# Optimization experiments

Hardware: AMD Instinct MI355X
Metric: run time of the kernel (lower is better)

The kernel has to match this reference:

```python
import jax, jax.numpy as jnp
import numpy as np

NQ = 16
DIM = 1 << NQ
NUM_BLOCKS = 2
TOTAL_PARAMS = 78  # per weight_shapes; only first 48 consumed by the circuit


def _apply_1q(state, w, U):
    # state: (B, DIM); U: (2,2) shared or (B,2,2) per-sample
    B = state.shape[0]
    s = state.reshape(B, 1 << w, 2, 1 << (NQ - 1 - w))
    if U.ndim == 2:
        out = jnp.einsum('ij,bljr->blir', U, s)
    else:
        out = jnp.einsum('bij,bljr->blir', U, s)
    return out.reshape(B, DIM)


def _apply_2q(state, a, b, U):
    # a < b always in this circuit; U: (4,4)
    B = state.shape[0]
    Ut = U.reshape(2, 2, 2, 2)
    s = state.reshape(B, 1 << a, 2, 1 << (b - a - 1), 2, 1 << (NQ - 1 - b))
    out = jnp.einsum('ijkl,bxkylz->bxiyjz', Ut, s)
    return out.reshape(B, DIM)


def _rx(t):
    c = jnp.cos(t / 2).astype(jnp.complex64)
    s = (-1j * jnp.sin(t / 2)).astype(jnp.complex64)
    return jnp.stack([jnp.stack([c, s], -1), jnp.stack([s, c], -1)], -2)


def _ry(t):
    c = jnp.cos(t / 2).astype(jnp.complex64)
    s = jnp.sin(t / 2).astype(jnp.complex64)
    return jnp.stack([jnp.stack([c, -s], -1), jnp.stack([s, c], -1)], -2)


def _rz(t):
    em = jnp.exp(-1j * t.astype(jnp.complex64) / 2)
    ep = jnp.exp(1j * t.astype(jnp.complex64) / 2)
    z = jnp.zeros_like(em)
    return jnp.stack([jnp.stack([em, z], -1), jnp.stack([z, ep], -1)], -2)


def _ising_xx(t):
    c = jnp.cos(t / 2).astype(jnp.complex64)
    m = (-1j * jnp.sin(t / 2)).astype(jnp.complex64)
    z = jnp.zeros((), jnp.complex64)
    return jnp.array([[c, z, z, m], [z, c, m, z], [z, m, c, z], [m, z, z, c]])


def _ising_yy(t):
    c = jnp.cos(t / 2).astype(jnp.complex64)
    m = (-1j * jnp.sin(t / 2)).astype(jnp.complex64)
    p = (1j * jnp.sin(t / 2)).astype(jnp.complex64)
    z = jnp.zeros((), jnp.complex64)
    return jnp.array([[c, z, z, p], [z, c, m, z], [z, m, c, z], [p, z, z, c]])


def _ising_zz(t):
    em = jnp.exp(-1j * t.astype(jnp.complex64) / 2)
    ep = jnp.exp(1j * t.astype(jnp.complex64) / 2)
    z = jnp.zeros((), jnp.complex64)
    return jnp.array([[em, z, z, z], [z, ep, z, z], [z, z, ep, z], [z, z, z, em]])


_H = (jnp.array([[1, 1], [1, -1]], jnp.complex64) / np.sqrt(2).astype(np.float32))
_CZ = jnp.diag(jnp.array([1, 1, 1, -1], jnp.complex64))
_CNOT = jnp.array([[1, 0, 0, 0], [0, 1, 0, 0], [0, 0, 0, 1], [0, 0, 1, 0]], jnp.complex64)


def _circuit(x, weights):
    B = x.shape[0]
    state = jnp.zeros((B, DIM), jnp.complex64).at[:, 0].set(1.0)
    # state preparation
    for q in range(NQ):
        state = _apply_1q(state, q, _H)
    for q in range(NQ - 1):
        state = _apply_2q(state, q, q + 1, _CZ)
    # feature encoding (per-sample angles)
    for q in range(NQ):
        ang = x[:, q]
        state = _apply_1q(state, q, _rx(ang))
        state = _apply_1q(state, q, _ry(ang))
        state = _apply_1q(state, q, _rz(ang))
    # conv + pool blocks
    qubits = list(range(NQ))
    idx = 0
    for _ in range(NUM_BLOCKS):
        npairs = len(qubits) // 2
        cw = weights[idx:idx + npairs * 3].reshape(npairs, 3)
        idx += npairs * 3
        for w_idx, i in enumerate(range(0, len(qubits) - 1, 2)):
            a, b = qubits[i], qubits[i + 1]
            state = _apply_2q(state, a, b, _ising_xx(cw[w_idx, 0]))
            state = _apply_2q(state, a, b, _ising_yy(cw[w_idx, 1]))
            state = _apply_2q(state, a, b, _ising_zz(cw[w_idx, 2]))
        nkeep = len(qubits) // 2
        pw = weights[idx:idx + nkeep]
        idx += nkeep
        new_q = []
        for i in range(0, len(qubits), 2):
            ctrl, tgt = qubits[i], qubits[i + 1]
            state = _apply_2q(state, ctrl, tgt, _CNOT)
            state = _apply_1q(state, ctrl, _ry(pw[i // 2]))
            new_q.append(ctrl)
        qubits = new_q
    # <Z> on surviving qubits [0,4,8,12]
    probs = state.real ** 2 + state.imag ** 2
    outs = []
    for q in qubits:
        p = probs.reshape(B, 1 << q, 2, -1)
        outs.append(p[:, :, 0, :].sum((1, 2)) - p[:, :, 1, :].sum((1, 2)))
    return jnp.stack(outs, -1)  # (B, 4)


def setup_inputs() -> dict:
    key = jax.random.key(0)
    k1, k2, k3 = jax.random.split(key, 3)
    x = jax.random.normal(k1, (32, NQ), jnp.float32)
    weights = 0.1 * jax.random.normal(k2, (TOTAL_PARAMS,), jnp.float32)
    W = 0.1 * jax.random.normal(k3, (9, 4), jnp.float32)  # Linear(4, 9)
    b = jnp.zeros((9,), jnp.float32)
    return {"x": x, "weights": weights, "W": W, "b": b}


def reference(x, weights, W, b):
    q_out = _circuit(x, weights)  # (B, 4) real
    return q_out @ W.T + b  # (B, 9)
```

## Files before the change

### kernel.cpp

```cpp
#include <hip/hip_runtime.h>
#include <math.h>


struct C { float x, y; };
__device__ __forceinline__ C operator+(C a, C b){ return {a.x+b.x, a.y+b.y}; }
__device__ __forceinline__ C operator-(C a, C b){ return {a.x-b.x, a.y-b.y}; }
__device__ __forceinline__ C cmul(C a, C b){ return { a.x*b.x - a.y*b.y, a.x*b.y + a.y*b.x }; }
__device__ __forceinline__ C cfma(C a, C b, C acc){
  acc.x = fmaf(a.x, b.x, fmaf(-a.y, b.y, acc.x));
  acc.y = fmaf(a.x, b.y, fmaf( a.y, b.x, acc.y));
  return acc;
}
__device__ __forceinline__ C cfmac(C a, C b, C acc){
  acc.x = fmaf(a.x, b.x, fmaf( a.y, b.y, acc.x));
  acc.y = fmaf(a.y, b.x, fmaf(-a.x, b.y, acc.y));
  return acc;
}
__device__ __forceinline__ C cscale(C a, float s){ return {a.x*s, a.y*s}; }

__global__ __launch_bounds__(256) void qk_all(const float* __restrict__ x,
                                              const float* __restrict__ w,
                                              const float* __restrict__ Wm,
                                              const float* __restrict__ bias,
                                              float* __restrict__ outp)
{
  __shared__ C G[12][16];
  __shared__ C uL[64];
  __shared__ C sV[1024];
  __shared__ C sT[256];
  __shared__ C sM[256];
  __shared__ C sDp[64];
  __shared__ C sDz[64];
  __shared__ float qv[4];

  const int tid = threadIdx.x;
  const int b   = blockIdx.x;

  {
    int p = tid >> 4;
    if (p < 12) {
      int idx = tid & 15, r = idx >> 2, c = idx & 3;
      float a0, a1, a2, ry;
      if (p < 8) { a0 = w[3*p];   a1 = w[3*p+1];  a2 = w[3*p+2];  ry = w[24+p]; }
      else { int n = p-8; a0 = w[32+3*n]; a1 = w[33+3*n]; a2 = w[34+3*n]; ry = w[44+n]; }
      float s0,c0,s1,c1,s2,c2,sr,cr;
      sincosf(0.5f*a0, &s0, &c0);
      sincosf(0.5f*a1, &s1, &c1);
      sincosf(0.5f*a2, &s2, &c2);
      sincosf(0.5f*ry, &sr, &cr);
      int rlo = r & 1, rhi = r >> 1;
      float d   = rlo ? fmaf(-s0, s1, c0*c1) : fmaf(s0, s1, c0*c1);
      float eps = rlo ? fmaf( c0, s1, c1*s0) : fmaf(-c0, s1, c1*s0);
      bool valid = rlo ? (c == 1 || c == 2) : (c == 0 || c == 3);
      bool sel   = rlo ? (c == 2) : (c == 3);
      float re, im;
      if (!sel) { re = rhi ?  sr*d : cr*d;  im = rhi ? -cr*eps :  sr*eps; }
      else      { re = rhi ?  cr*d : -sr*d; im = rhi ? -sr*eps : -cr*eps; }
      float zi = rlo ? s2 : -s2;
      C val;
      if (valid) val = { fmaf(re, c2, -im*zi), fmaf(re, zi, im*c2) };
      else       val = {0.f, 0.f};
      G[p][idx] = val;
    } else if (tid >= 192 && tid < 208) {
      int q = tid - 192;
      float h = 0.5f * x[b*16 + q];
      float s, c;
      sincosf(h, &s, &c);
      C em = {c,-s}, ep = {c,s};
      C A00 = { c*c,  s*s}, A01 = {-c*s, -c*s};
      C A10 = { c*s, -c*s}, A11 = { c*c, -s*s};
      uL[q*4+0] = cmul(em, A00);
      uL[q*4+1] = cmul(em, A01);
      uL[q*4+2] = cmul(ep, A10);
      uL[q*4+3] = cmul(ep, A11);
    }
  }
  __syncthreads();

  {
    int lp = tid >> 4, lc = tid & 15;
    int p3=(lp>>3)&1, p2=(lp>>2)&1, p1=(lp>>1)&1, p0=lp&1;
    int l3=(lc>>3)&1, l2=(lc>>2)&1, l1=(lc>>1)&1, l0=lc&1;
    for (int n=0;n<4;n++){
      C acc{0,0};
      #pragma unroll
      for (int m3=0;m3<2;m3++)
      #pragma unroll
      for (int m1=0;m1<2;m1++){
        C g2 = G[8+n]  [(p3*2+p1)*4 + (m3*2+m1)];
        C ga = G[2*n]  [(m3*2+p2)*4 + (l3*2+l2)];
        C gb = G[2*n+1][(m1*2+p0)*4 + (l1*2+l0)];
        acc = cfma(g2, cmul(ga, gb), acc);
      }
      sV[n*256 + lp*16 + lc] = acc;
    }
  }
  if (tid < 64) {
    int n = tid >> 4, s = tid & 15;
    int t0 = (s>>3)&1;
    C u0 = uL[(4*n)*4 + t0*2 + 0], u1 = uL[(4*n)*4 + t0*2 + 1];
    C P00=u0, P01=u0, P10=u1, P11={-u1.x,-u1.y};
    #pragma unroll
    for (int i=1;i<4;i++){
      int t = (s >> (3-i)) & 1;
      int q = 4*n + i;
      C v0 = uL[q*4 + t*2 + 0], v1 = uL[q*4 + t*2 + 1];
      C b00, b01, b10, b11;
      if (n == 3 && i == 3) { b00=v0; b01={0,0}; b10=v1; b11={0,0}; }
      else { b00=v0; b01=v0; b10=v1; b11={-v1.x,-v1.y}; }
      C n00 = cfma(P01, b10, cmul(P00, b00));
      C n01 = cfma(P01, b11, cmul(P00, b01));
      C n10 = cfma(P11, b10, cmul(P10, b00));
      C n11 = cfma(P11, b11, cmul(P10, b01));
      P00=n00; P01=n01; P10=n10; P11=n11;
    }
    int base = tid << 2;
    sT[base+0]=P00; sT[base+1]=P01; sT[base+2]=P10; sT[base+3]=P11;
  }
  __syncthreads();

  {
    int n = tid >> 6, s = (tid >> 2) & 15, ab = tid & 3;
    const C* vr = &sV[n*256 + s*16];
    const C* tn = &sT[(n<<6) + ab];
    C acc{0,0};
    #pragma unroll
    for (int k=0;k<16;k++) acc = cfma(vr[k], tn[k<<2], acc);
    sM[tid] = acc;
  }
  __syncthreads();

  if (tid < 64) {
    int n = tid >> 4, p = tid & 15;
    int a=(p>>3)&1, a2=(p>>2)&1, bb=(p>>1)&1, b2=p&1;
    const C* mn = &sM[n<<6];
    C Slo{0,0}, Shi{0,0};
    #pragma unroll
    for (int s=0;s<8;s++)  Slo = cfmac(mn[(s<<2)+(a<<1)+bb], mn[(s<<2)+(a2<<1)+b2], Slo);
    #pragma unroll
    for (int s=8;s<16;s++) Shi = cfmac(mn[(s<<2)+(a<<1)+bb], mn[(s<<2)+(a2<<1)+b2], Shi);
    sDp[tid] = Slo + Shi;
    sDz[tid] = Slo - Shi;
  }
  __syncthreads();

  if (tid < 4) {
    int o = tid;
    C v0={1,0}, v1={1,0}, v2={1,0}, v3={1,0};
    #pragma unroll
    for (int n=0;n<3;n++){
      const C* D = (n==o) ? &sDz[n<<4] : &sDp[n<<4];
      C n0{0,0}, n1{0,0}, n2{0,0}, n3{0,0};
      n0 = cfma(v0, D[ 0], n0); n0 = cfma(v1, D[ 4], n0); n0 = cfma(v2, D[ 8], n0); n0 = cfma(v3, D[12], n0);
      n1 = cfma(v0, D[ 1], n1); n1 = cfma(v1, D[ 5], n1); n1 = cfma(v2, D[ 9], n1); n1 = cfma(v3, D[13], n1);
      n2 = cfma(v0, D[ 2], n2); n2 = cfma(v1, D[ 6], n2); n2 = cfma(v2, D[10], n2); n2 = cfma(v3, D[14], n2);
      n3 = cfma(v0, D[ 3], n3); n3 = cfma(v1, D[ 7], n3); n3 = cfma(v2, D[11], n3); n3 = cfma(v3, D[15], n3);
      v0=n0; v1=n1; v2=n2; v3=n3;
    }
    const C* D3 = (o==3) ? &sDz[3<<4] : &sDp[3<<4];
    C e{0,0};
    e = cfma(v0, D3[ 0], e); e = cfma(v1, D3[ 4], e);
    e = cfma(v2, D3[ 8], e); e = cfma(v3, D3[12], e);
    qv[o] = e.x * (1.0f/65536.0f);
  }
  __syncthreads();

  if (tid < 9) {
    float acc = bias[tid];
    #pragma unroll
    for (int k=0;k<4;k++) acc = fmaf(qv[k], Wm[tid*4+k], acc);
    outp[b*9 + tid] = acc;
  }
}

extern "C" void kernel_launch(void* const* d_in, const int* in_sizes, int n_in,
                              void* d_out, int out_size, void* d_ws, size_t ws_size,
                              hipStream_t stream)
{
  (void)in_sizes; (void)n_in; (void)out_size; (void)d_ws; (void)ws_size;
  const float* x    = (const float*)d_in[0];
  const float* w    = (const float*)d_in[1];
  const float* Wm   = (const float*)d_in[2];
  const float* bias = (const float*)d_in[3];
  float* outp = (float*)d_out;

  qk_all<<<32, 256, 0, stream>>>(x, w, Wm, bias, outp);
}
```

Measured before the change: 9.584 us.

## Factor per-block contraction into half-products and parallelize reduction stages

Replaces the 1024-entry sV tensor plus product-state sT contraction with a factored scheme. It builds 128 half-block partial products sH, then forms sM directly from the G[8+n] gate and pairs of half products, cutting arithmetic and shared memory. The density reduction is split across 128 threads by low/high half, and the final chain runs on 16 lanes with shuffles instead of 4 serial threads. It also switches to fast __sincosf intrinsics, which trades some accuracy for cheaper transcendentals.

```diff
diff --git a/kernel.cpp b/kernel.cpp
--- a/kernel.cpp
+++ b/kernel.cpp
@@ -16,7 +16,6 @@
   acc.y = fmaf(a.y, b.x, fmaf(-a.x, b.y, acc.y));
   return acc;
 }
-__device__ __forceinline__ C cscale(C a, float s){ return {a.x*s, a.y*s}; }
 
 __global__ __launch_bounds__(256) void qk_all(const float* __restrict__ x,
                                               const float* __restrict__ w,
@@ -26,11 +25,10 @@
 {
   __shared__ C G[12][16];
   __shared__ C uL[64];
-  __shared__ C sV[1024];
-  __shared__ C sT[256];
+  __shared__ C sH[128];
   __shared__ C sM[256];
-  __shared__ C sDp[64];
-  __shared__ C sDz[64];
+  __shared__ C sSlo[64];
+  __shared__ C sShi[64];
   __shared__ float qv[4];
 
   const int tid = threadIdx.x;
@@ -44,10 +42,10 @@
       if (p < 8) { a0 = w[3*p];   a1 = w[3*p+1];  a2 = w[3*p+2];  ry = w[24+p]; }
       else { int n = p-8; a0 = w[32+3*n]; a1 = w[33+3*n]; a2 = w[34+3*n]; ry = w[44+n]; }
       float s0,c0,s1,c1,s2,c2,sr,cr;
-      sincosf(0.5f*a0, &s0, &c0);
-      sincosf(0.5f*a1, &s1, &c1);
-      sincosf(0.5f*a2, &s2, &c2);
-      sincosf(0.5f*ry, &sr, &cr);
+      __sincosf(0.5f*a0, &s0, &c0);
+      __sincosf(0.5f*a1, &s1, &c1);
+      __sincosf(0.5f*a2, &s2, &c2);
+      __sincosf(0.5f*ry, &sr, &cr);
       int rlo = r & 1, rhi = r >> 1;
       float d   = rlo ? fmaf(-s0, s1, c0*c1) : fmaf(s0, s1, c0*c1);
       float eps = rlo ? fmaf( c0, s1, c1*s0) : fmaf(-c0, s1, c1*s0);
@@ -65,7 +63,7 @@
       int q = tid - 192;
       float h = 0.5f * x[b*16 + q];
       float s, c;
-      sincosf(h, &s, &c);
+      __sincosf(h, &s, &c);
       C em = {c,-s}, ep = {c,s};
       C A00 = { c*c,  s*s}, A01 = {-c*s, -c*s};
       C A10 = { c*s, -c*s}, A11 = { c*c, -s*s};
@@ -77,91 +75,94 @@
   }
   __syncthreads();
 
-  {
-    int lp = tid >> 4, lc = tid & 15;
-    int p3=(lp>>3)&1, p2=(lp>>2)&1, p1=(lp>>1)&1, p0=lp&1;
-    int l3=(lc>>3)&1, l2=(lc>>2)&1, l1=(lc>>1)&1, l0=lc&1;
-    for (int n=0;n<4;n++){
-      C acc{0,0};
-      #pragma unroll
-      for (int m3=0;m3<2;m3++)
-      #pragma unroll
-      for (int m1=0;m1<2;m1++){
-        C g2 = G[8+n]  [(p3*2+p1)*4 + (m3*2+m1)];
-        C ga = G[2*n]  [(m3*2+p2)*4 + (l3*2+l2)];
-        C gb = G[2*n+1][(m1*2+p0)*4 + (l1*2+l0)];
-        acc = cfma(g2, cmul(ga, gb), acc);
+  if (tid < 128) {
+    int n = tid >> 5, side = (tid >> 4) & 1, u = (tid >> 2) & 3;
+    int a = (tid >> 1) & 1, bb = tid & 1;
+    int q1 = 4*n + 2*side;
+    bool chat = (n == 3 && side == 1);
+    float t1 = a ? -1.f : 1.f;
+    float coef = (chat || !bb) ? t1 : -t1;
+    bool zero = chat && bb;
+    const C* g1 = &G[2*n + side][u*4];
+    C acc{0,0};
+    #pragma unroll
+    for (int v=0; v<4; v++){
+      C pv{0,0};
+      if (!zero) {
+        int thi = v >> 1, tlo = v & 1;
+        C u1a = uL[q1*4 + thi*2 + a];
+        C u20 = uL[q1*4 + 4 + tlo*2 + 0];
+        C u21 = uL[q1*4 + 4 + tlo*2 + 1];
+        C inner = { fmaf(coef, u21.x, u20.x), fmaf(coef, u21.y, u20.y) };
+        pv = cmul(u1a, inner);
       }
-      sV[n*256 + lp*16 + lc] = acc;
+      acc = cfma(g1[v], pv, acc);
     }
-  }
-  if (tid < 64) {
-    int n = tid >> 4, s = tid & 15;
-    int t0 = (s>>3)&1;
-    C u0 = uL[(4*n)*4 + t0*2 + 0], u1 = uL[(4*n)*4 + t0*2 + 1];
-    C P00=u0, P01=u0, P10=u1, P11={-u1.x,-u1.y};
-    #pragma unroll
-    for (int i=1;i<4;i++){
-      int t = (s >> (3-i)) & 1;
-      int q = 4*n + i;
-      C v0 = uL[q*4 + t*2 + 0], v1 = uL[q*4 + t*2 + 1];
-      C b00, b01, b10, b11;
-      if (n == 3 && i == 3) { b00=v0; b01={0,0}; b10=v1; b11={0,0}; }
-      else { b00=v0; b01=v0; b10=v1; b11={-v1.x,-v1.y}; }
-      C n00 = cfma(P01, b10, cmul(P00, b00));
-      C n01 = cfma(P01, b11, cmul(P00, b01));
-      C n10 = cfma(P11, b10, cmul(P10, b00));
-      C n11 = cfma(P11, b11, cmul(P10, b01));
-      P00=n00; P01=n01; P10=n10; P11=n11;
-    }
-    int base = tid << 2;
-    sT[base+0]=P00; sT[base+1]=P01; sT[base+2]=P10; sT[base+3]=P11;
+    sH[tid] = acc;
   }
   __syncthreads();
 
   {
-    int n = tid >> 6, s = (tid >> 2) & 15, ab = tid & 3;
-    const C* vr = &sV[n*256 + s*16];
-    const C* tn = &sT[(n<<6) + ab];
+    int n = tid >> 6, s = (tid >> 2) & 15;
+    int a = (tid >> 1) & 1, bb = tid & 1;
+    int s3=(s>>3)&1, s2b=(s>>2)&1, s1=(s>>1)&1, s0=s&1;
+    const C* g2 = &G[8+n][(s3*2+s1)*4];
+    const C* hn = &sH[n*32];
     C acc{0,0};
     #pragma unroll
-    for (int k=0;k<16;k++) acc = cfma(vr[k], tn[k<<2], acc);
+    for (int m3=0;m3<2;m3++)
+    #pragma unroll
+    for (int m1=0;m1<2;m1++){
+      const C* Ha = &hn[(m3*2+s2b)*4];
+      const C* Hb = &hn[16 + (m1*2+s0)*4];
+      C X = cmul(Ha[a*2+0], Hb[bb]) + cmul(Ha[a*2+1], Hb[2+bb]);
+      acc = cfma(g2[m3*2+m1], X, acc);
+    }
     sM[tid] = acc;
   }
   __syncthreads();
 
-  if (tid < 64) {
-    int n = tid >> 4, p = tid & 15;
+  if (tid < 128) {
+    int h = tid >> 6, idx = tid & 63;
+    int n = idx >> 4, p = idx & 15;
     int a=(p>>3)&1, a2=(p>>2)&1, bb=(p>>1)&1, b2=p&1;
     const C* mn = &sM[n<<6];
-    C Slo{0,0}, Shi{0,0};
+    C S{0,0};
     #pragma unroll
-    for (int s=0;s<8;s++)  Slo = cfmac(mn[(s<<2)+(a<<1)+bb], mn[(s<<2)+(a2<<1)+b2], Slo);
-    #pragma unroll
-    for (int s=8;s<16;s++) Shi = cfmac(mn[(s<<2)+(a<<1)+bb], mn[(s<<2)+(a2<<1)+b2], Shi);
-    sDp[tid] = Slo + Shi;
-    sDz[tid] = Slo - Shi;
+    for (int s=0;s<8;s++){
+      int sc = (h*8 + s) << 2;
+      S = cfmac(mn[sc+(a<<1)+bb], mn[sc+(a2<<1)+b2], S);
+    }
+    if (h) sShi[idx] = S; else sSlo[idx] = S;
   }
   __syncthreads();
 
-  if (tid < 4) {
-    int o = tid;
-    C v0={1,0}, v1={1,0}, v2={1,0}, v3={1,0};
+  if (tid < 16) {
+    int o = tid >> 2, j = tid & 3;
+    int grp = tid & ~3;
+    C v = {1.f, 0.f};
     #pragma unroll
-    for (int n=0;n<3;n++){
-      const C* D = (n==o) ? &sDz[n<<4] : &sDp[n<<4];
-      C n0{0,0}, n1{0,0}, n2{0,0}, n3{0,0};
-      n0 = cfma(v0, D[ 0], n0); n0 = cfma(v1, D[ 4], n0); n0 = cfma(v2, D[ 8], n0); n0 = cfma(v3, D[12], n0);
-      n1 = cfma(v0, D[ 1], n1); n1 = cfma(v1, D[ 5], n1); n1 = cfma(v2, D[ 9], n1); n1 = cfma(v3, D[13], n1);
-      n2 = cfma(v0, D[ 2], n2); n2 = cfma(v1, D[ 6], n2); n2 = cfma(v2, D[10], n2); n2 = cfma(v3, D[14], n2);
-      n3 = cfma(v0, D[ 3], n3); n3 = cfma(v1, D[ 7], n3); n3 = cfma(v2, D[11], n3); n3 = cfma(v3, D[15], n3);
-      v0=n0; v1=n1; v2=n2; v3=n3;
+    for (int n=0; n<3; n++){
+      float sgn = (n==o) ? -1.f : 1.f;
+      C nv{0,0};
+      #pragma unroll
+      for (int i=0;i<4;i++){
+        C vi = { __shfl(v.x, grp+i), __shfl(v.y, grp+i) };
+        int di = n*16 + i*4 + j;
+        C D = { fmaf(sgn, sShi[di].x, sSlo[di].x),
+                fmaf(sgn, sShi[di].y, sSlo[di].y) };
+        nv = cfma(vi, D, nv);
+      }
+      v = nv;
     }
-    const C* D3 = (o==3) ? &sDz[3<<4] : &sDp[3<<4];
-    C e{0,0};
-    e = cfma(v0, D3[ 0], e); e = cfma(v1, D3[ 4], e);
-    e = cfma(v2, D3[ 8], e); e = cfma(v3, D3[12], e);
-    qv[o] = e.x * (1.0f/65536.0f);
+    float sgn3 = (o==3) ? -1.f : 1.f;
+    int di = 48 + j*4;
+    C D3 = { fmaf(sgn3, sShi[di].x, sSlo[di].x),
+             fmaf(sgn3, sShi[di].y, sSlo[di].y) };
+    C p = cmul(v, D3);
+    p.x += __shfl_xor(p.x, 1);
+    p.x += __shfl_xor(p.x, 2);
+    if (j == 0) qv[o] = p.x * (1.0f/65536.0f);
   }
   __syncthreads();
 
```

Result: slower. 16.45 us (+71.7%).
